# Kernel tuning notes

Measured on AMD Instinct MI355X. Metric: run time of the kernel, lower is better.

Reference implementation:

```python
import math
import jax, jax.numpy as jnp
import numpy as np

B, TQ, TK = 16, 2048, 1024
D_DEC, D_ENC, D_ATT = 256, 256, 128
WINDOW_SIZE = 3


def setup_inputs() -> dict:
    key = jax.random.key(0)
    ks = jax.random.split(key, 11)
    s = 0.02
    return {
        "query": jax.random.normal(ks[0], (B, TQ, D_DEC), jnp.float32),
        "keys": jax.random.normal(ks[1], (B, TK, D_ENC), jnp.float32),
        "values": jax.random.normal(ks[2], (B, TK, D_ENC), jnp.float32),
        "Wq": jax.random.normal(ks[3], (D_ATT, D_DEC), jnp.float32) * s,
        "bq": jax.random.normal(ks[4], (D_ATT,), jnp.float32) * s,
        "Wk": jax.random.normal(ks[5], (D_ATT, D_ENC), jnp.float32) * s,
        "bk": jax.random.normal(ks[6], (D_ATT,), jnp.float32) * s,
        "Wv": jax.random.normal(ks[7], (D_ATT, D_ENC), jnp.float32) * s,
        "bv": jax.random.normal(ks[8], (D_ATT,), jnp.float32) * s,
        "Wo": jax.random.normal(ks[9], (D_DEC, D_ATT), jnp.float32) * s,
        "bo": jax.random.normal(ks[10], (D_DEC,), jnp.float32) * s,
        "prev_max_attention_idx": 100,
    }


def reference(query, keys, values, Wq, bq, Wk, bk, Wv, bv, Wo, bo,
              prev_max_attention_idx):
    residual = query
    q = query @ Wq.T + bq            # [B, Tq, A]
    k = keys @ Wk.T + bk             # [B, Tk, A]
    v = values @ Wv.T + bv           # [B, Tk, A]
    scores = jnp.einsum('bqa,bka->bqk', q, k)  # [B, Tq, Tk]
    Tk = scores.shape[-1]
    col = jnp.arange(Tk)
    # mask [:prev] if prev > 0, and [prev + window :] if in range
    masked = (col < prev_max_attention_idx) | (col >= prev_max_attention_idx + WINDOW_SIZE)
    scores = jnp.where(masked[None, None, :], -jnp.inf, scores)
    attn = jax.nn.softmax(scores, axis=-1)
    attn_scores = attn
    # dropout_prob = 0.0 -> identity
    ctx = jnp.einsum('bqk,bka->bqa', attn, v)
    s = v.shape[1]
    ctx = ctx * (s * math.sqrt(1.0 / s))  # == sqrt(Tk)
    out = (ctx @ Wo.T + bo + residual) * math.sqrt(0.5)
    return (out, attn_scores)
```

## Files before the change

### kernel.cpp

```cpp
#include <hip/hip_runtime.h>
#include <math.h>

#define BATCH 16
#define TQL   2048
#define TKL   1024
#define DDEC  256
#define DENC  256
#define DATT  128
#define WIN   3

#define WS_KQ 0
#define WS_VO (48*DDEC)
#define WS_KB (2*48*DDEC)

#define NZBLK 2048

__global__ __launch_bounds__(256) void pre_and_zero(
    const float* __restrict__ keys, const float* __restrict__ values,
    const float* __restrict__ Wk, const float* __restrict__ bk,
    const float* __restrict__ Wv, const float* __restrict__ bv,
    const float* __restrict__ Wq, const float* __restrict__ bq,
    const float* __restrict__ Wo, const int* __restrict__ pidx,
    float* __restrict__ ws, float* __restrict__ attn)
{
    const int t = threadIdx.x;

    if (blockIdx.x >= 48) {
        const int zb = blockIdx.x - 48;
        float4* p = (float4*)attn + (size_t)zb * 4096;
        const float4 z4 = make_float4(0.0f, 0.0f, 0.0f, 0.0f);
        #pragma unroll
        for (int i = 0; i < 16; ++i) p[i * 256 + t] = z4;
        return;
    }

    const int blk = blockIdx.x;
    const int b = blk / WIN, j = blk % WIN;
    const int prev = pidx[0];
    const int col = prev + j;
    const bool valid = (col >= 0) && (col < TKL);

    __shared__ float ksh[DENC];
    __shared__ float vsh[DENC];
    __shared__ float kwsh[DATT];
    __shared__ float vwsh[DATT];

    {
        size_t base = ((size_t)b * TKL + (valid ? col : 0)) * DENC + t;
        ksh[t] = valid ? keys[base]   : 0.0f;
        vsh[t] = valid ? values[base] : 0.0f;
    }
    __syncthreads();

    if (t < DATT) {
        const float4* wrow = (const float4*)(Wk + (size_t)t * DENC);
        float acc = 0.0f;
        #pragma unroll 8
        for (int k4 = 0; k4 < DENC / 4; ++k4) {
            float4 w = wrow[k4];
            acc += w.x * ksh[k4*4+0] + w.y * ksh[k4*4+1]
                 + w.z * ksh[k4*4+2] + w.w * ksh[k4*4+3];
        }
        kwsh[t] = acc + bk[t];
    } else {
        const int c = t - DATT;
        const float4* wrow = (const float4*)(Wv + (size_t)c * DENC);
        float acc = 0.0f;
        #pragma unroll 8
        for (int k4 = 0; k4 < DENC / 4; ++k4) {
            float4 w = wrow[k4];
            acc += w.x * vsh[k4*4+0] + w.y * vsh[k4*4+1]
                 + w.z * vsh[k4*4+2] + w.w * vsh[k4*4+3];
        }
        vwsh[c] = acc + bv[c];
    }
    __syncthreads();

    float accq = 0.0f, acco = 0.0f;
    const float4* worow = (const float4*)(Wo + (size_t)t * DATT);
    #pragma unroll 4
    for (int c4 = 0; c4 < DATT / 4; ++c4) {
        float4 w = worow[c4];
        acco += w.x * vwsh[c4*4+0] + w.y * vwsh[c4*4+1]
              + w.z * vwsh[c4*4+2] + w.w * vwsh[c4*4+3];
        accq += kwsh[c4*4+0] * Wq[(size_t)(c4*4+0) * DDEC + t]
              + kwsh[c4*4+1] * Wq[(size_t)(c4*4+1) * DDEC + t]
              + kwsh[c4*4+2] * Wq[(size_t)(c4*4+2) * DDEC + t]
              + kwsh[c4*4+3] * Wq[(size_t)(c4*4+3) * DDEC + t];
    }
    ws[WS_KQ + blk * DDEC + t] = accq;
    ws[WS_VO + blk * DDEC + t] = acco;

    if (t < 64) {
        float pb = bq[t] * kwsh[t] + bq[t + 64] * kwsh[t + 64];
        #pragma unroll
        for (int off = 32; off > 0; off >>= 1) pb += __shfl_xor(pb, off, 64);
        if (t == 0) ws[WS_KB + blk] = pb;
    }
}

__device__ __forceinline__ float winval(int ww, float w0, float w1, float w2) {
    float v = (ww == 0) ? w0 : ((ww == 1) ? w1 : ((ww == 2) ? w2 : 0.0f));
    return (ww >= 0 && ww < WIN) ? v : 0.0f;
}

__global__ __launch_bounds__(256) void attn_out(
    const float* __restrict__ query, const float* __restrict__ bo,
    const int* __restrict__ pidx, const float* __restrict__ ws,
    float* __restrict__ out, float* __restrict__ attn)
{
    const float* kq = ws + WS_KQ;
    const float* vo = ws + WS_VO;
    const float* kb = ws + WS_KB;
    const int prev = pidx[0];

    const int t    = threadIdx.x;
    const int lane = t & 63;
    const int wid  = t >> 6;
    const int g    = lane >> 4;
    const int sub  = lane & 15;
    const int row  = blockIdx.x * 16 + wid * 4 + g;
    const int b    = row >> 11;
    const int base = b * WIN;

    const float4* q4p = (const float4*)query + (size_t)row * 64;
    const float4 q0 = q4p[ 0 + sub];
    const float4 q1 = q4p[16 + sub];
    const float4 q2 = q4p[32 + sub];
    const float4 q3 = q4p[48 + sub];

    const float4* kqp0 = (const float4*)kq + (size_t)(base + 0) * 64;
    const float4* kqp1 = (const float4*)kq + (size_t)(base + 1) * 64;
    const float4* kqp2 = (const float4*)kq + (size_t)(base + 2) * 64;

    float p0, p1, p2;
    {
        float4 k0, k1, k2;
        k0 = kqp0[ 0 + sub]; k1 = kqp1[ 0 + sub]; k2 = kqp2[ 0 + sub];
        p0  = q0.x*k0.x + q0.y*k0.y + q0.z*k0.z + q0.w*k0.w;
        p1  = q0.x*k1.x + q0.y*k1.y + q0.z*k1.z + q0.w*k1.w;
        p2  = q0.x*k2.x + q0.y*k2.y + q0.z*k2.z + q0.w*k2.w;
        k0 = kqp0[16 + sub]; k1 = kqp1[16 + sub]; k2 = kqp2[16 + sub];
        p0 += q1.x*k0.x + q1.y*k0.y + q1.z*k0.z + q1.w*k0.w;
        p1 += q1.x*k1.x + q1.y*k1.y + q1.z*k1.z + q1.w*k1.w;
        p2 += q1.x*k2.x + q1.y*k2.y + q1.z*k2.z + q1.w*k2.w;
        k0 = kqp0[32 + sub]; k1 = kqp1[32 + sub]; k2 = kqp2[32 + sub];
        p0 += q2.x*k0.x + q2.y*k0.y + q2.z*k0.z + q2.w*k0.w;
        p1 += q2.x*k1.x + q2.y*k1.y + q2.z*k1.z + q2.w*k1.w;
        p2 += q2.x*k2.x + q2.y*k2.y + q2.z*k2.z + q2.w*k2.w;
        k0 = kqp0[48 + sub]; k1 = kqp1[48 + sub]; k2 = kqp2[48 + sub];
        p0 += q3.x*k0.x + q3.y*k0.y + q3.z*k0.z + q3.w*k0.w;
        p1 += q3.x*k1.x + q3.y*k1.y + q3.z*k1.z + q3.w*k1.w;
        p2 += q3.x*k2.x + q3.y*k2.y + q3.z*k2.z + q3.w*k2.w;
    }
    #pragma unroll
    for (int off = 8; off > 0; off >>= 1) {
        p0 += __shfl_xor(p0, off, 64);
        p1 += __shfl_xor(p1, off, 64);
        p2 += __shfl_xor(p2, off, 64);
    }

    float s0 = p0 + kb[base + 0];
    float s1 = p1 + kb[base + 1];
    float s2 = p2 + kb[base + 2];

    const bool v0 = (prev + 0 >= 0) && (prev + 0 < TKL);
    const bool v1 = (prev + 1 >= 0) && (prev + 1 < TKL);
    const bool v2 = (prev + 2 >= 0) && (prev + 2 < TKL);
    const float NEG = -3.0e38f;
    if (!v0) s0 = NEG;
    if (!v1) s1 = NEG;
    if (!v2) s2 = NEG;

    const float m  = fmaxf(s0, fmaxf(s1, s2));
    const float e0 = v0 ? __expf(s0 - m) : 0.0f;
    const float e1 = v1 ? __expf(s1 - m) : 0.0f;
    const float e2 = v2 ? __expf(s2 - m) : 0.0f;
    const float inv = 1.0f / (e0 + e1 + e2);
    const float w0 = e0 * inv, w1 = e1 * inv, w2 = e2 * inv;

    const float CTX_SCALE = 32.0f;
    const float RSQ2 = 0.70710678118654752f;

    const float4* vop0 = (const float4*)vo + (size_t)(base + 0) * 64;
    const float4* vop1 = (const float4*)vo + (size_t)(base + 1) * 64;
    const float4* vop2 = (const float4*)vo + (size_t)(base + 2) * 64;
    const float4* bo4p = (const float4*)bo;
    float4* orow = (float4*)(out + (size_t)row * DDEC);

    #pragma unroll
    for (int k = 0; k < 4; ++k) {
        const float4 x0 = vop0[k * 16 + sub];
        const float4 x1 = vop1[k * 16 + sub];
        const float4 x2 = vop2[k * 16 + sub];
        const float4 bb = bo4p[k * 16 + sub];
        const float4 qq = (k == 0) ? q0 : (k == 1) ? q1 : (k == 2) ? q2 : q3;
        float4 o;
        o.x = (CTX_SCALE * (w0*x0.x + w1*x1.x + w2*x2.x) + bb.x + qq.x) * RSQ2;
        o.y = (CTX_SCALE * (w0*x0.y + w1*x1.y + w2*x2.y) + bb.y + qq.y) * RSQ2;
        o.z = (CTX_SCALE * (w0*x0.z + w1*x1.z + w2*x2.z) + bb.z + qq.z) * RSQ2;
        o.w = (CTX_SCALE * (w0*x0.w + w1*x1.w + w2*x2.w) + bb.w + qq.w) * RSQ2;
        orow[k * 16 + sub] = o;
    }

    int lo = prev < 0 ? 0 : prev;
    int hi = prev + (WIN - 1) > TKL - 1 ? TKL - 1 : prev + (WIN - 1);
    if (lo <= hi) {
        const int f0 = lo >> 2, f1 = hi >> 2;
        float4* arow = (float4*)(attn + (size_t)row * TKL);
        if ((f0 & 15) == sub) {
            const int c0 = f0 * 4;
            float4 pz;
            pz.x = winval(c0 + 0 - prev, w0, w1, w2);
            pz.y = winval(c0 + 1 - prev, w0, w1, w2);
            pz.z = winval(c0 + 2 - prev, w0, w1, w2);
            pz.w = winval(c0 + 3 - prev, w0, w1, w2);
            arow[f0] = pz;
        }
        if (f1 != f0 && (f1 & 15) == sub) {
            const int c0 = f1 * 4;
            float4 pz;
            pz.x = winval(c0 + 0 - prev, w0, w1, w2);
            pz.y = winval(c0 + 1 - prev, w0, w1, w2);
            pz.z = winval(c0 + 2 - prev, w0, w1, w2);
            pz.w = winval(c0 + 3 - prev, w0, w1, w2);
            arow[f1] = pz;
        }
    }
}

extern "C" void kernel_launch(void* const* d_in, const int* in_sizes, int n_in,
                              void* d_out, int out_size, void* d_ws, size_t ws_size,
                              hipStream_t stream)
{
    const float* query  = (const float*)d_in[0];
    const float* keys   = (const float*)d_in[1];
    const float* values = (const float*)d_in[2];
    const float* Wq     = (const float*)d_in[3];
    const float* bq     = (const float*)d_in[4];
    const float* Wk     = (const float*)d_in[5];
    const float* bk     = (const float*)d_in[6];
    const float* Wv     = (const float*)d_in[7];
    const float* bv     = (const float*)d_in[8];
    const float* Wo     = (const float*)d_in[9];
    const float* bo     = (const float*)d_in[10];
    const int*   pidx   = (const int*)d_in[11];

    float* ws   = (float*)d_ws;
    float* out  = (float*)d_out;
    float* attn = out + (size_t)BATCH * TQL * DDEC;

    pre_and_zero<<<48 + NZBLK, 256, 0, stream>>>(keys, values, Wk, bk, Wv, bv,
                                                 Wq, bq, Wo, pidx, ws, attn);
    attn_out<<<BATCH * TQL / 16, 256, 0, stream>>>(query, bo, pidx, ws, out, attn);
}
```

Measured before the change: 41.95 us.

## Stage window vectors in LDS, process two rows per thread, use nontemporal zero stores

The attention-output kernel now copies the per-batch projected key/value window vectors, the output bias and the key biases into shared memory once per block. Each thread then handles two query rows, so every block covers 32 rows and the grid is halved. The zero-fill of the attention matrix now uses nontemporal stores with smaller blocks and twice as many of them, to avoid polluting the cache on the 128MB write stream. The costs are an added __syncthreads and shared-memory traffic, and the kernel stays bound by the output write bandwidth.

New measurement: 47.97 us. +14.4%, slower.

```diff
diff --git a/kernel.cpp b/kernel.cpp
--- a/kernel.cpp
+++ b/kernel.cpp
@@ -9,11 +9,13 @@
 #define DATT  128
 #define WIN   3
 
+typedef float f32x4 __attribute__((ext_vector_type(4)));
+
 #define WS_KQ 0
 #define WS_VO (48*DDEC)
 #define WS_KB (2*48*DDEC)
 
-#define NZBLK 2048
+#define NZBLK 4096
 
 __global__ __launch_bounds__(256) void pre_and_zero(
     const float* __restrict__ keys, const float* __restrict__ values,
@@ -27,10 +29,11 @@
 
     if (blockIdx.x >= 48) {
         const int zb = blockIdx.x - 48;
-        float4* p = (float4*)attn + (size_t)zb * 4096;
-        const float4 z4 = make_float4(0.0f, 0.0f, 0.0f, 0.0f);
+        f32x4* p = (f32x4*)attn + (size_t)zb * 2048;
+        const f32x4 z4 = (f32x4)(0.0f);
         #pragma unroll
-        for (int i = 0; i < 16; ++i) p[i * 256 + t] = z4;
+        for (int i = 0; i < 8; ++i)
+            __builtin_nontemporal_store(z4, p + i * 256 + t);
         return;
     }
 
@@ -104,51 +107,32 @@
     return (ww >= 0 && ww < WIN) ? v : 0.0f;
 }
 
-__global__ __launch_bounds__(256) void attn_out(
-    const float* __restrict__ query, const float* __restrict__ bo,
-    const int* __restrict__ pidx, const float* __restrict__ ws,
+__device__ __forceinline__ void process_row(
+    int row, int sub, int prev, int f0, int f1,
+    const float4 q0, const float4 q1, const float4 q2, const float4 q3,
+    const float* kqsh, const float* vosh, const float* bosh, const float* kbsh,
     float* __restrict__ out, float* __restrict__ attn)
 {
-    const float* kq = ws + WS_KQ;
-    const float* vo = ws + WS_VO;
-    const float* kb = ws + WS_KB;
-    const int prev = pidx[0];
-
-    const int t    = threadIdx.x;
-    const int lane = t & 63;
-    const int wid  = t >> 6;
-    const int g    = lane >> 4;
-    const int sub  = lane & 15;
-    const int row  = blockIdx.x * 16 + wid * 4 + g;
-    const int b    = row >> 11;
-    const int base = b * WIN;
-
-    const float4* q4p = (const float4*)query + (size_t)row * 64;
-    const float4 q0 = q4p[ 0 + sub];
-    const float4 q1 = q4p[16 + sub];
-    const float4 q2 = q4p[32 + sub];
-    const float4 q3 = q4p[48 + sub];
-
-    const float4* kqp0 = (const float4*)kq + (size_t)(base + 0) * 64;
-    const float4* kqp1 = (const float4*)kq + (size_t)(base + 1) * 64;
-    const float4* kqp2 = (const float4*)kq + (size_t)(base + 2) * 64;
+    const float4* kq4 = (const float4*)kqsh;
+    const float4* vo4 = (const float4*)vosh;
+    const float4* bo4 = (const float4*)bosh;
 
     float p0, p1, p2;
     {
         float4 k0, k1, k2;
-        k0 = kqp0[ 0 + sub]; k1 = kqp1[ 0 + sub]; k2 = kqp2[ 0 + sub];
+        k0 = kq4[ 0 + sub]; k1 = kq4[ 64 + sub]; k2 = kq4[128 + sub];
         p0  = q0.x*k0.x + q0.y*k0.y + q0.z*k0.z + q0.w*k0.w;
         p1  = q0.x*k1.x + q0.y*k1.y + q0.z*k1.z + q0.w*k1.w;
         p2  = q0.x*k2.x + q0.y*k2.y + q0.z*k2.z + q0.w*k2.w;
-        k0 = kqp0[16 + sub]; k1 = kqp1[16 + sub]; k2 = kqp2[16 + sub];
+        k0 = kq4[16 + sub]; k1 = kq4[ 80 + sub]; k2 = kq4[144 + sub];
         p0 += q1.x*k0.x + q1.y*k0.y + q1.z*k0.z + q1.w*k0.w;
         p1 += q1.x*k1.x + q1.y*k1.y + q1.z*k1.z + q1.w*k1.w;
         p2 += q1.x*k2.x + q1.y*k2.y + q1.z*k2.z + q1.w*k2.w;
-        k0 = kqp0[32 + sub]; k1 = kqp1[32 + sub]; k2 = kqp2[32 + sub];
+        k0 = kq4[32 + sub]; k1 = kq4[ 96 + sub]; k2 = kq4[160 + sub];
         p0 += q2.x*k0.x + q2.y*k0.y + q2.z*k0.z + q2.w*k0.w;
         p1 += q2.x*k1.x + q2.y*k1.y + q2.z*k1.z + q2.w*k1.w;
         p2 += q2.x*k2.x + q2.y*k2.y + q2.z*k2.z + q2.w*k2.w;
-        k0 = kqp0[48 + sub]; k1 = kqp1[48 + sub]; k2 = kqp2[48 + sub];
+        k0 = kq4[48 + sub]; k1 = kq4[112 + sub]; k2 = kq4[176 + sub];
         p0 += q3.x*k0.x + q3.y*k0.y + q3.z*k0.z + q3.w*k0.w;
         p1 += q3.x*k1.x + q3.y*k1.y + q3.z*k1.z + q3.w*k1.w;
         p2 += q3.x*k2.x + q3.y*k2.y + q3.z*k2.z + q3.w*k2.w;
@@ -160,9 +144,9 @@
         p2 += __shfl_xor(p2, off, 64);
     }
 
-    float s0 = p0 + kb[base + 0];
-    float s1 = p1 + kb[base + 1];
-    float s2 = p2 + kb[base + 2];
+    float s0 = p0 + kbsh[0];
+    float s1 = p1 + kbsh[1];
+    float s2 = p2 + kbsh[2];
 
     const bool v0 = (prev + 0 >= 0) && (prev + 0 < TKL);
     const bool v1 = (prev + 1 >= 0) && (prev + 1 < TKL);
@@ -182,18 +166,13 @@
     const float CTX_SCALE = 32.0f;
     const float RSQ2 = 0.70710678118654752f;
 
-    const float4* vop0 = (const float4*)vo + (size_t)(base + 0) * 64;
-    const float4* vop1 = (const float4*)vo + (size_t)(base + 1) * 64;
-    const float4* vop2 = (const float4*)vo + (size_t)(base + 2) * 64;
-    const float4* bo4p = (const float4*)bo;
     float4* orow = (float4*)(out + (size_t)row * DDEC);
-
     #pragma unroll
     for (int k = 0; k < 4; ++k) {
-        const float4 x0 = vop0[k * 16 + sub];
-        const float4 x1 = vop1[k * 16 + sub];
-        const float4 x2 = vop2[k * 16 + sub];
-        const float4 bb = bo4p[k * 16 + sub];
+        const float4 x0 = vo4[k * 16 + sub];
+        const float4 x1 = vo4[k * 16 + 64 + sub];
+        const float4 x2 = vo4[k * 16 + 128 + sub];
+        const float4 bb = bo4[k * 16 + sub];
         const float4 qq = (k == 0) ? q0 : (k == 1) ? q1 : (k == 2) ? q2 : q3;
         float4 o;
         o.x = (CTX_SCALE * (w0*x0.x + w1*x1.x + w2*x2.x) + bb.x + qq.x) * RSQ2;
@@ -203,10 +182,7 @@
         orow[k * 16 + sub] = o;
     }
 
-    int lo = prev < 0 ? 0 : prev;
-    int hi = prev + (WIN - 1) > TKL - 1 ? TKL - 1 : prev + (WIN - 1);
-    if (lo <= hi) {
-        const int f0 = lo >> 2, f1 = hi >> 2;
+    if (f0 >= 0) {
         float4* arow = (float4*)(attn + (size_t)row * TKL);
         if ((f0 & 15) == sub) {
             const int c0 = f0 * 4;
@@ -227,6 +203,53 @@
             arow[f1] = pz;
         }
     }
+}
+
+__global__ __launch_bounds__(256) void attn_out(
+    const float* __restrict__ query, const float* __restrict__ bo,
+    const int* __restrict__ pidx, const float* __restrict__ ws,
+    float* __restrict__ out, float* __restrict__ attn)
+{
+    const int t   = threadIdx.x;
+    const int G   = t >> 4;
+    const int sub = t & 15;
+    const int blk = blockIdx.x;
+    const int b   = blk >> 6;
+    const int base = b * WIN;
+    const int prev = pidx[0];
+
+    const int rowA = blk * 32 + G;
+    const int rowB = rowA + 16;
+
+    const float4* qA = (const float4*)query + (size_t)rowA * 64;
+    const float4* qB = (const float4*)query + (size_t)rowB * 64;
+    const float4 a0 = qA[ 0 + sub], a1 = qA[16 + sub],
+                 a2 = qA[32 + sub], a3 = qA[48 + sub];
+    const float4 b0 = qB[ 0 + sub], b1 = qB[16 + sub],
+                 b2 = qB[32 + sub], b3 = qB[48 + sub];
+
+    __shared__ float kqsh[3 * DDEC];
+    __shared__ float vosh[3 * DDEC];
+    __shared__ float bosh[DDEC];
+    __shared__ float kbsh[WIN];
+    #pragma unroll
+    for (int j = 0; j < 3; ++j) {
+        kqsh[j * DDEC + t] = ws[WS_KQ + (base + j) * DDEC + t];
+        vosh[j * DDEC + t] = ws[WS_VO + (base + j) * DDEC + t];
+    }
+    bosh[t] = bo[t];
+    if (t < WIN) kbsh[t] = ws[WS_KB + base + t];
+    __syncthreads();
+
+    int lo = prev < 0 ? 0 : prev;
+    int hi = prev + (WIN - 1) > TKL - 1 ? TKL - 1 : prev + (WIN - 1);
+    int f0 = -1, f1 = -1;
+    if (lo <= hi) { f0 = lo >> 2; f1 = hi >> 2; }
+
+    process_row(rowA, sub, prev, f0, f1, a0, a1, a2, a3,
+                kqsh, vosh, bosh, kbsh, out, attn);
+    process_row(rowB, sub, prev, f0, f1, b0, b1, b2, b3,
+                kqsh, vosh, bosh, kbsh, out, attn);
 }
 
 extern "C" void kernel_launch(void* const* d_in, const int* in_sizes, int n_in,
@@ -252,5 +275,5 @@
 
     pre_and_zero<<<48 + NZBLK, 256, 0, stream>>>(keys, values, Wk, bk, Wv, bv,
                                                  Wq, bq, Wo, pidx, ws, attn);
-    attn_out<<<BATCH * TQL / 16, 256, 0, stream>>>(query, bo, pidx, ws, out, attn);
-}
+    attn_out<<<BATCH * TQL / 32, 256, 0, stream>>>(query, bo, pidx, ws, out, attn);
+}
```
